# Performance work log

Measured on AMD Instinct MI355X. Metric: run time of the kernel, lower is better.

## Reference

```python
import jax, jax.numpy as jnp
import numpy as np

B, N, FIN, D1, D2 = 4096, 64, 256, 512, 128
NEG = -10000000.0


def setup_inputs() -> dict:
    key = jax.random.key(0)
    ks = jax.random.split(key, 12)
    s = lambda fan_in: 1.0 / np.sqrt(fan_in)
    return {
        "obs_x": jax.random.normal(ks[0], (B, FIN), jnp.float32),
        "others": jax.random.normal(ks[1], (B, N, FIN), jnp.float32),
        "action_mask": jax.random.randint(ks[2], (B, D2), 0, 2, jnp.int32),
        "W1": jax.random.normal(ks[3], (FIN, D1), jnp.float32) * s(FIN),
        "b1": jnp.zeros((D1,), jnp.float32),
        "W2": jax.random.normal(ks[4], (2 * D1, D2), jnp.float32) * s(2 * D1),
        "b2": jnp.zeros((D2,), jnp.float32),
        "W3": jax.random.normal(ks[5], (2 * D1, D2), jnp.float32) * s(2 * D1),
        "b3": jnp.zeros((D2,), jnp.float32),
        "W4": jax.random.normal(ks[6], (D2, 1), jnp.float32) * s(D2),
        "b4": jnp.zeros((1,), jnp.float32),
    }


def reference(obs_x, others, action_mask, W1, b1, W2, b2, W3, b3, W4, b4):
    # shared fc1 projection of self obs and other agents' obs
    x = obs_x @ W1 + b1                       # [B, D1]
    y = jnp.einsum("bnf,fd->bnd", others, W1) + b1  # [B, N, D1]
    # single-query dot-product attention over other agents
    alpha = jnp.einsum("bd,bnd->bn", x, y) / jnp.sqrt(jnp.float32(x.shape[-1]))
    beta = jax.nn.softmax(alpha, axis=-1)     # [B, N]
    c = jnp.einsum("bn,bnd->bd", beta, y)     # context [B, D1]
    out = jnp.concatenate([x, c], axis=-1)    # [B, 2*D1]
    out1 = jax.nn.softmax(out @ W2 + b2, axis=-1)  # policy branch (softmax then mask, as in source)
    mask = action_mask.astype(out1.dtype)
    logits = out1 + NEG * (1.0 - mask)
    value = (out @ W3 + b3) @ W4 + b4         # [B, 1] value head (stored as self._value_out)
    del value  # forward() returns only the masked logits
    return logits.reshape(-1, D2)
```

## Files before the change

kernel.cpp:

```cpp
#include <hip/hip_runtime.h>
#include <hip/hip_bf16.h>


typedef unsigned short u16;
typedef __bf16 bf16x8 __attribute__((ext_vector_type(8)));
typedef float f32x4 __attribute__((ext_vector_type(4)));

#define FIN 256
#define D1  512
#define D2  128
#define NNA 64
#define NEGV -10000000.0f

__device__ __forceinline__ float bf2f(u16 u) {
  unsigned int i = ((unsigned int)u) << 16;
  return __builtin_bit_cast(float, i);
}
__device__ __forceinline__ u16 f2bf(float f) {
  unsigned int i = __builtin_bit_cast(unsigned int, f);
  return (u16)((i + 0x7FFFu + ((i >> 16) & 1u)) >> 16);
}
__device__ __forceinline__ bf16x8 ld_frag_g(const u16* p) {
  return __builtin_bit_cast(bf16x8, *(const uint4*)p);
}
__device__ __forceinline__ bf16x8 ld_frag_f32(const float* p) {
  float4 a = *(const float4*)p, b = *(const float4*)(p + 4);
  u16 s[8];
  s[0] = f2bf(a.x); s[1] = f2bf(a.y); s[2] = f2bf(a.z); s[3] = f2bf(a.w);
  s[4] = f2bf(b.x); s[5] = f2bf(b.y); s[6] = f2bf(b.z); s[7] = f2bf(b.w);
  return __builtin_bit_cast(bf16x8, *(uint4*)s);
}

__global__ __launch_bounds__(256) void k_prep(const float* __restrict__ W1,
                                              const float* __restrict__ W2,
                                              u16* __restrict__ W1p,
                                              u16* __restrict__ W2p,
                                              u16* __restrict__ W1tp) {
  int tid = blockIdx.x * 256 + threadIdx.x;
  if (tid < 131072) {
    int idx = tid;
    int j = idx & 7, lane = (idx >> 3) & 63, nt = (idx >> 9) & 31, kt = idx >> 14;
    int k = kt * 32 + (lane >> 4) * 8 + j;
    int n = nt * 16 + (lane & 15);
    W1p[idx] = f2bf(W1[k * D1 + n]);
  } else if (tid < 163840) {
    int idx = tid - 131072;
    int j = idx & 7, lane = (idx >> 3) & 63, nt = (idx >> 9) & 7, kt = idx >> 12;
    int k = kt * 32 + (lane >> 4) * 8 + j;
    int n = nt * 16 + (lane & 15);
    W2p[idx] = f2bf(W2[k * D2 + n]);
  } else {
    int idx = tid - 163840;
    int j = idx & 7, lane = (idx >> 3) & 63, nt = (idx >> 9) & 15, kt = idx >> 13;
    int k = kt * 32 + (lane >> 4) * 8 + j;
    int n = nt * 16 + (lane & 15);
    W1tp[idx] = f2bf(W1[n * D1 + k]);
  }
}

__global__ __launch_bounds__(64) void k_x(const float* __restrict__ obs,
                                          const u16* __restrict__ W1p,
                                          const float* __restrict__ pb1,
                                          u16* __restrict__ outw) {
  const int lane = threadIdx.x & 63;
  const int q = lane >> 4, c0 = lane & 15;
  const int m0 = blockIdx.x * 32;
  const int ntg0 = blockIdx.y * 8;

  f32x4 acc[2][8];
#pragma unroll
  for (int a = 0; a < 2; ++a)
#pragma unroll
    for (int c = 0; c < 8; ++c) acc[a][c] = (f32x4){0.f, 0.f, 0.f, 0.f};

#pragma unroll 1
  for (int kt = 0; kt < 8; ++kt) {
    bf16x8 afr[2], bfr[8];
#pragma unroll
    for (int mt = 0; mt < 2; ++mt)
      afr[mt] = ld_frag_f32(obs + (m0 + mt * 16 + c0) * FIN + kt * 32 + q * 8);
#pragma unroll
    for (int nt = 0; nt < 8; ++nt)
      bfr[nt] = ld_frag_g(W1p + ((kt * 32 + ntg0 + nt) * 64 + lane) * 8);
#pragma unroll
    for (int mt = 0; mt < 2; ++mt)
#pragma unroll
      for (int nt = 0; nt < 8; ++nt)
        acc[mt][nt] = __builtin_amdgcn_mfma_f32_16x16x32_bf16(afr[mt], bfr[nt], acc[mt][nt], 0, 0, 0);
  }

#pragma unroll
  for (int nt = 0; nt < 8; ++nt) {
    const int n = (ntg0 + nt) * 16 + c0;
    const float bias = pb1[n];
#pragma unroll
    for (int mt = 0; mt < 2; ++mt)
#pragma unroll
      for (int i = 0; i < 4; ++i) {
        const int row = m0 + mt * 16 + q * 4 + i;
        outw[row * 512 + n] = f2bf(acc[mt][nt][i] + bias);
      }
  }
}

__global__ __launch_bounds__(64) void k_z(const u16* __restrict__ outw,
                                          const u16* __restrict__ W1tp,
                                          float* __restrict__ zbuf) {
  const int lane = threadIdx.x & 63;
  const int q = lane >> 4, c0 = lane & 15;
  const int m0 = blockIdx.x * 32;
  const int ntg0 = blockIdx.y * 8;

  f32x4 acc[2][8];
#pragma unroll
  for (int a = 0; a < 2; ++a)
#pragma unroll
    for (int c = 0; c < 8; ++c) acc[a][c] = (f32x4){0.f, 0.f, 0.f, 0.f};

#pragma unroll 1
  for (int kt = 0; kt < 16; ++kt) {
    bf16x8 afr[2], bfr[8];
#pragma unroll
    for (int mt = 0; mt < 2; ++mt)
      afr[mt] = ld_frag_g(outw + (m0 + mt * 16 + c0) * 512 + kt * 32 + q * 8);
#pragma unroll
    for (int nt = 0; nt < 8; ++nt)
      bfr[nt] = ld_frag_g(W1tp + ((kt * 16 + ntg0 + nt) * 64 + lane) * 8);
#pragma unroll
    for (int mt = 0; mt < 2; ++mt)
#pragma unroll
      for (int nt = 0; nt < 8; ++nt)
        acc[mt][nt] = __builtin_amdgcn_mfma_f32_16x16x32_bf16(afr[mt], bfr[nt], acc[mt][nt], 0, 0, 0);
  }

#pragma unroll
  for (int nt = 0; nt < 8; ++nt) {
    const int n = (ntg0 + nt) * 16 + c0;
#pragma unroll
    for (int mt = 0; mt < 2; ++mt)
#pragma unroll
      for (int i = 0; i < 4; ++i) {
        const int row = m0 + mt * 16 + q * 4 + i;
        zbuf[row * 256 + n] = acc[mt][nt][i];
      }
  }
}

__global__ __launch_bounds__(256, 4) void k_attn(const float* __restrict__ others,
                                                 const float* __restrict__ zbuf,
                                                 u16* __restrict__ obarb) {
  __shared__ float s_alpha[64];
  __shared__ float s_beta[64];
  __shared__ float s_part[1024];

  const int tid = threadIdx.x;
  const int b = blockIdx.x;
  const int w = tid >> 6, l = tid & 63;
  const float* src = others + (size_t)b * (NNA * FIN);

  const float4 z4 = *(const float4*)(zbuf + b * 256 + 4 * l);

  float4 o4[16];
#pragma unroll
  for (int r = 0; r < 16; ++r)
    o4[r] = *(const float4*)(src + (w * 16 + r) * 256 + 4 * l);

#pragma unroll
  for (int r = 0; r < 16; ++r) {
    float s = o4[r].x * z4.x + o4[r].y * z4.y + o4[r].z * z4.z + o4[r].w * z4.w;
    s += __shfl_xor(s, 1);  s += __shfl_xor(s, 2);  s += __shfl_xor(s, 4);
    s += __shfl_xor(s, 8);  s += __shfl_xor(s, 16); s += __shfl_xor(s, 32);
    if (l == r) s_alpha[w * 16 + r] = s * 0.04419417382415922f;
  }
  __syncthreads();

  if (tid < 64) {
    float v = s_alpha[tid];
    float mx = v;
#pragma unroll
    for (int off = 1; off < 64; off <<= 1) mx = fmaxf(mx, __shfl_xor(mx, off));
    float e = __expf(v - mx);
    float se = e;
#pragma unroll
    for (int off = 1; off < 64; off <<= 1) se += __shfl_xor(se, off);
    s_beta[tid] = e / se;
  }
  __syncthreads();

  float4 p = (float4){0.f, 0.f, 0.f, 0.f};
#pragma unroll
  for (int r = 0; r < 16; ++r) {
    const float bb = s_beta[w * 16 + r];
    p.x += bb * o4[r].x; p.y += bb * o4[r].y; p.z += bb * o4[r].z; p.w += bb * o4[r].w;
  }
  *(float4*)(&s_part[w * 256 + 4 * l]) = p;
  __syncthreads();

  const float v = s_part[tid] + s_part[tid + 256] + s_part[tid + 512] + s_part[tid + 768];
  obarb[(size_t)b * 256 + tid] = f2bf(v);
}

__global__ __launch_bounds__(128) void k_tail(const u16* __restrict__ outw,
                                              const u16* __restrict__ obarb,
                                              const u16* __restrict__ W1p,
                                              const float* __restrict__ pb1,
                                              const u16* __restrict__ W2p,
                                              const float* __restrict__ pb2,
                                              const int* __restrict__ mask,
                                              float* __restrict__ out) {
  __shared__ __align__(16) u16 c_s[16 * 520];
  __shared__ float s_mx[2][16];
  __shared__ float s_se[2][16];

  const int tid = threadIdx.x;
  const int w = tid >> 6, lane = tid & 63;
  const int q = lane >> 4, c0 = lane & 15;
  const int m0 = blockIdx.x * 16;

  {
    f32x4 acc[16];
#pragma unroll
    for (int c = 0; c < 16; ++c) acc[c] = (f32x4){0.f, 0.f, 0.f, 0.f};

#pragma unroll 1
    for (int kt = 0; kt < 8; ++kt) {
      bf16x8 afr = ld_frag_g(obarb + (m0 + c0) * 256 + kt * 32 + q * 8);
      bf16x8 bfr[16];
#pragma unroll
      for (int nt = 0; nt < 16; ++nt)
        bfr[nt] = ld_frag_g(W1p + ((kt * 32 + w * 16 + nt) * 64 + lane) * 8);
#pragma unroll
      for (int nt = 0; nt < 16; ++nt)
        acc[nt] = __builtin_amdgcn_mfma_f32_16x16x32_bf16(afr, bfr[nt], acc[nt], 0, 0, 0);
    }

#pragma unroll
    for (int nt = 0; nt < 16; ++nt) {
      const int n = w * 256 + nt * 16 + c0;
      const float bias = pb1[n];
#pragma unroll
      for (int i = 0; i < 4; ++i)
        c_s[(q * 4 + i) * 520 + n] = f2bf(acc[nt][i] + bias);
    }
  }
  __syncthreads();

  f32x4 acc[4];
#pragma unroll
  for (int c = 0; c < 4; ++c) acc[c] = (f32x4){0.f, 0.f, 0.f, 0.f};

#pragma unroll 1
  for (int kt = 0; kt < 16; ++kt) {
    bf16x8 afr = ld_frag_g(outw + (m0 + c0) * 512 + kt * 32 + q * 8);
    bf16x8 bfr[4];
#pragma unroll
    for (int nt = 0; nt < 4; ++nt)
      bfr[nt] = ld_frag_g(W2p + ((kt * 8 + w * 4 + nt) * 64 + lane) * 8);
#pragma unroll
    for (int nt = 0; nt < 4; ++nt)
      acc[nt] = __builtin_amdgcn_mfma_f32_16x16x32_bf16(afr, bfr[nt], acc[nt], 0, 0, 0);
  }
#pragma unroll 1
  for (int kt = 0; kt < 16; ++kt) {
    bf16x8 afr = __builtin_bit_cast(bf16x8, *(const uint4*)(c_s + c0 * 520 + kt * 32 + q * 8));
    bf16x8 bfr[4];
#pragma unroll
    for (int nt = 0; nt < 4; ++nt)
      bfr[nt] = ld_frag_g(W2p + (((kt + 16) * 8 + w * 4 + nt) * 64 + lane) * 8);
#pragma unroll
    for (int nt = 0; nt < 4; ++nt)
      acc[nt] = __builtin_amdgcn_mfma_f32_16x16x32_bf16(afr, bfr[nt], acc[nt], 0, 0, 0);
  }

  float b2f[4];
#pragma unroll
  for (int nt = 0; nt < 4; ++nt) b2f[nt] = pb2[(w * 4 + nt) * 16 + c0];

  float vv[4][4];
#pragma unroll
  for (int i = 0; i < 4; ++i) {
    float mx = -3.0e38f;
#pragma unroll
    for (int nt = 0; nt < 4; ++nt) { vv[i][nt] = acc[nt][i] + b2f[nt]; mx = fmaxf(mx, vv[i][nt]); }
    mx = fmaxf(mx, __shfl_xor(mx, 1)); mx = fmaxf(mx, __shfl_xor(mx, 2));
    mx = fmaxf(mx, __shfl_xor(mx, 4)); mx = fmaxf(mx, __shfl_xor(mx, 8));
    if (c0 == 0) s_mx[w][q * 4 + i] = mx;
  }
  __syncthreads();

#pragma unroll
  for (int i = 0; i < 4; ++i) {
    const int r = q * 4 + i;
    const float mx = fmaxf(s_mx[0][r], s_mx[1][r]);
    float se = 0.f;
#pragma unroll
    for (int nt = 0; nt < 4; ++nt) { vv[i][nt] = __expf(vv[i][nt] - mx); se += vv[i][nt]; }
    se += __shfl_xor(se, 1); se += __shfl_xor(se, 2);
    se += __shfl_xor(se, 4); se += __shfl_xor(se, 8);
    if (c0 == 0) s_se[w][q * 4 + i] = se;
  }
  __syncthreads();

#pragma unroll
  for (int i = 0; i < 4; ++i) {
    const int r = q * 4 + i;
    const int row = m0 + r;
    const float inv = 1.f / (s_se[0][r] + s_se[1][r]);
#pragma unroll
    for (int nt = 0; nt < 4; ++nt) {
      const int col = (w * 4 + nt) * 16 + c0;
      float p = fminf(fmaxf(vv[i][nt] * inv, 0.f), 1.f);
      float o = mask[row * D2 + col] ? p : (p + NEGV);
      out[row * D2 + col] = o;
    }
  }
}

extern "C" void kernel_launch(void* const* d_in, const int* in_sizes, int n_in,
                              void* d_out, int out_size, void* d_ws, size_t ws_size,
                              hipStream_t stream) {
  const float* obs = (const float*)d_in[0];
  const float* oth = (const float*)d_in[1];
  const int*   msk = (const int*)d_in[2];
  const float* W1  = (const float*)d_in[3];
  const float* b1  = (const float*)d_in[4];
  const float* W2  = (const float*)d_in[5];
  const float* b2  = (const float*)d_in[6];
  float* out = (float*)d_out;

  char* ws = (char*)d_ws;
  u16*   W1p   = (u16*)ws;
  u16*   W2p   = (u16*)(ws + 262144);
  u16*   W1tp  = (u16*)(ws + 327680);
  u16*   outw  = (u16*)(ws + 589824);
  float* zbuf  = (float*)(ws + 4784128);
  u16*   obarb = (u16*)(ws + 8978432);

  k_prep<<<1152, 256, 0, stream>>>(W1, W2, W1p, W2p, W1tp);
  k_x<<<dim3(128, 4), 64, 0, stream>>>(obs, W1p, b1, outw);
  k_z<<<dim3(128, 2), 64, 0, stream>>>(outw, W1tp, zbuf);
  k_attn<<<4096, 256, 0, stream>>>(oth, zbuf, obarb);
  k_tail<<<256, 128, 0, stream>>>(outw, obarb, W1p, b1, W2p, b2, msk, out);
}
```

Before: 427.2 us.

## Fuse x and z projections into one kernel and streamline attention reductions

Merges the x = obs@W1 and z = x@W1^T GEMMs into a single kernel. It keeps the bf16 x tile in shared memory so z no longer re-reads outw from global memory, and it saves one launch. In the attention kernel, the 16 separate full-wave shuffle reductions become a transposed butterfly reduction that needs far fewer shuffles. The others tensor is now read with nontemporal loads. The fused kernel uses 16-row tiles with 4 waves, which changes the parallelism and the reuse of W1 loads per block.

```diff
diff --git a/kernel.cpp b/kernel.cpp
--- a/kernel.cpp
+++ b/kernel.cpp
@@ -29,6 +29,9 @@
   s[0] = f2bf(a.x); s[1] = f2bf(a.y); s[2] = f2bf(a.z); s[3] = f2bf(a.w);
   s[4] = f2bf(b.x); s[5] = f2bf(b.y); s[6] = f2bf(b.z); s[7] = f2bf(b.w);
   return __builtin_bit_cast(bf16x8, *(uint4*)s);
+}
+__device__ __forceinline__ f32x4 ldnt(const float* p) {
+  return __builtin_nontemporal_load((const f32x4*)p);
 }
 
 __global__ __launch_bounds__(256) void k_prep(const float* __restrict__ W1,
@@ -58,91 +61,76 @@
   }
 }
 
-__global__ __launch_bounds__(64) void k_x(const float* __restrict__ obs,
-                                          const u16* __restrict__ W1p,
-                                          const float* __restrict__ pb1,
-                                          u16* __restrict__ outw) {
-  const int lane = threadIdx.x & 63;
+__global__ __launch_bounds__(256) void k_xz(const float* __restrict__ obs,
+                                            const u16* __restrict__ W1p,
+                                            const u16* __restrict__ W1tp,
+                                            const float* __restrict__ pb1,
+                                            u16* __restrict__ outw,
+                                            float* __restrict__ zbuf) {
+  __shared__ __align__(16) u16 x_s[16 * 520];
+
+  const int tid = threadIdx.x;
+  const int w = tid >> 6, lane = tid & 63;
   const int q = lane >> 4, c0 = lane & 15;
-  const int m0 = blockIdx.x * 32;
-  const int ntg0 = blockIdx.y * 8;
-
-  f32x4 acc[2][8];
-#pragma unroll
-  for (int a = 0; a < 2; ++a)
-#pragma unroll
-    for (int c = 0; c < 8; ++c) acc[a][c] = (f32x4){0.f, 0.f, 0.f, 0.f};
-
-#pragma unroll 1
-  for (int kt = 0; kt < 8; ++kt) {
-    bf16x8 afr[2], bfr[8];
-#pragma unroll
-    for (int mt = 0; mt < 2; ++mt)
-      afr[mt] = ld_frag_f32(obs + (m0 + mt * 16 + c0) * FIN + kt * 32 + q * 8);
-#pragma unroll
-    for (int nt = 0; nt < 8; ++nt)
-      bfr[nt] = ld_frag_g(W1p + ((kt * 32 + ntg0 + nt) * 64 + lane) * 8);
-#pragma unroll
-    for (int mt = 0; mt < 2; ++mt)
+  const int m0 = blockIdx.x * 16;
+  const int ntg0 = w * 8;
+
+  {
+    f32x4 acc[8];
+#pragma unroll
+    for (int c = 0; c < 8; ++c) acc[c] = (f32x4){0.f, 0.f, 0.f, 0.f};
+
+#pragma unroll 1
+    for (int kt = 0; kt < 8; ++kt) {
+      bf16x8 afr = ld_frag_f32(obs + (m0 + c0) * FIN + kt * 32 + q * 8);
+      bf16x8 bfr[8];
 #pragma unroll
       for (int nt = 0; nt < 8; ++nt)
-        acc[mt][nt] = __builtin_amdgcn_mfma_f32_16x16x32_bf16(afr[mt], bfr[nt], acc[mt][nt], 0, 0, 0);
-  }
-
-#pragma unroll
-  for (int nt = 0; nt < 8; ++nt) {
-    const int n = (ntg0 + nt) * 16 + c0;
-    const float bias = pb1[n];
-#pragma unroll
-    for (int mt = 0; mt < 2; ++mt)
+        bfr[nt] = ld_frag_g(W1p + ((kt * 32 + ntg0 + nt) * 64 + lane) * 8);
+#pragma unroll
+      for (int nt = 0; nt < 8; ++nt)
+        acc[nt] = __builtin_amdgcn_mfma_f32_16x16x32_bf16(afr, bfr[nt], acc[nt], 0, 0, 0);
+    }
+
+#pragma unroll
+    for (int nt = 0; nt < 8; ++nt) {
+      const int n = (ntg0 + nt) * 16 + c0;
+      const float bias = pb1[n];
 #pragma unroll
       for (int i = 0; i < 4; ++i) {
-        const int row = m0 + mt * 16 + q * 4 + i;
-        outw[row * 512 + n] = f2bf(acc[mt][nt][i] + bias);
+        const int r = q * 4 + i;
+        const u16 hv = f2bf(acc[nt][i] + bias);
+        outw[(m0 + r) * 512 + n] = hv;
+        x_s[r * 520 + n] = hv;
       }
-  }
-}
-
-__global__ __launch_bounds__(64) void k_z(const u16* __restrict__ outw,
-                                          const u16* __restrict__ W1tp,
-                                          float* __restrict__ zbuf) {
-  const int lane = threadIdx.x & 63;
-  const int q = lane >> 4, c0 = lane & 15;
-  const int m0 = blockIdx.x * 32;
-  const int ntg0 = blockIdx.y * 8;
-
-  f32x4 acc[2][8];
-#pragma unroll
-  for (int a = 0; a < 2; ++a)
-#pragma unroll
-    for (int c = 0; c < 8; ++c) acc[a][c] = (f32x4){0.f, 0.f, 0.f, 0.f};
-
-#pragma unroll 1
-  for (int kt = 0; kt < 16; ++kt) {
-    bf16x8 afr[2], bfr[8];
-#pragma unroll
-    for (int mt = 0; mt < 2; ++mt)
-      afr[mt] = ld_frag_g(outw + (m0 + mt * 16 + c0) * 512 + kt * 32 + q * 8);
-#pragma unroll
-    for (int nt = 0; nt < 8; ++nt)
-      bfr[nt] = ld_frag_g(W1tp + ((kt * 16 + ntg0 + nt) * 64 + lane) * 8);
-#pragma unroll
-    for (int mt = 0; mt < 2; ++mt)
-#pragma unroll
-      for (int nt = 0; nt < 8; ++nt)
-        acc[mt][nt] = __builtin_amdgcn_mfma_f32_16x16x32_bf16(afr[mt], bfr[nt], acc[mt][nt], 0, 0, 0);
-  }
-
-#pragma unroll
-  for (int nt = 0; nt < 8; ++nt) {
-    const int n = (ntg0 + nt) * 16 + c0;
-#pragma unroll
-    for (int mt = 0; mt < 2; ++mt)
-#pragma unroll
-      for (int i = 0; i < 4; ++i) {
-        const int row = m0 + mt * 16 + q * 4 + i;
-        zbuf[row * 256 + n] = acc[mt][nt][i];
-      }
+    }
+  }
+  __syncthreads();
+
+  {
+    f32x4 acc[4];
+#pragma unroll
+    for (int c = 0; c < 4; ++c) acc[c] = (f32x4){0.f, 0.f, 0.f, 0.f};
+
+#pragma unroll 1
+    for (int kt = 0; kt < 16; ++kt) {
+      bf16x8 afr = __builtin_bit_cast(bf16x8, *(const uint4*)(x_s + c0 * 520 + kt * 32 + q * 8));
+      bf16x8 bfr[4];
+#pragma unroll
+      for (int nt = 0; nt < 4; ++nt)
+        bfr[nt] = ld_frag_g(W1tp + ((kt * 16 + w * 4 + nt) * 64 + lane) * 8);
+#pragma unroll
+      for (int nt = 0; nt < 4; ++nt)
+        acc[nt] = __builtin_amdgcn_mfma_f32_16x16x32_bf16(afr, bfr[nt], acc[nt], 0, 0, 0);
+    }
+
+#pragma unroll
+    for (int nt = 0; nt < 4; ++nt) {
+      const int n = (w * 4 + nt) * 16 + c0;
+#pragma unroll
+      for (int i = 0; i < 4; ++i)
+        zbuf[(m0 + q * 4 + i) * 256 + n] = acc[nt][i];
+    }
   }
 }
 
@@ -158,28 +146,43 @@
   const int w = tid >> 6, l = tid & 63;
   const float* src = others + (size_t)b * (NNA * FIN);
 
-  const float4 z4 = *(const float4*)(zbuf + b * 256 + 4 * l);
-
-  float4 o4[16];
+  const f32x4 z4 = *(const f32x4*)(zbuf + b * 256 + 4 * l);
+
+  f32x4 o4[16];
 #pragma unroll
   for (int r = 0; r < 16; ++r)
-    o4[r] = *(const float4*)(src + (w * 16 + r) * 256 + 4 * l);
-
-#pragma unroll
-  for (int r = 0; r < 16; ++r) {
-    float s = o4[r].x * z4.x + o4[r].y * z4.y + o4[r].z * z4.z + o4[r].w * z4.w;
-    s += __shfl_xor(s, 1);  s += __shfl_xor(s, 2);  s += __shfl_xor(s, 4);
-    s += __shfl_xor(s, 8);  s += __shfl_xor(s, 16); s += __shfl_xor(s, 32);
-    if (l == r) s_alpha[w * 16 + r] = s * 0.04419417382415922f;
-  }
+    o4[r] = ldnt(src + (w * 16 + r) * 256 + 4 * l);
+
+  float v[16];
+#pragma unroll
+  for (int r = 0; r < 16; ++r)
+    v[r] = o4[r][0] * z4[0] + o4[r][1] * z4[1] + o4[r][2] * z4[2] + o4[r][3] * z4[3];
+
+#pragma unroll
+  for (int k = 0; k < 4; ++k) {
+    const int m = 1 << k;
+    const int half = 8 >> k;
+    const bool hi = (l & m) != 0;
+#pragma unroll
+    for (int i = 0; i < half; ++i) {
+      float a = v[i], bv = v[i + half];
+      float send = hi ? a : bv;
+      float keep = hi ? bv : a;
+      v[i] = keep + __shfl_xor(send, m);
+    }
+  }
+  v[0] += __shfl_xor(v[0], 16);
+  v[0] += __shfl_xor(v[0], 32);
+  const int rr = ((l & 1) << 3) | (((l >> 1) & 1) << 2) | (((l >> 2) & 1) << 1) | ((l >> 3) & 1);
+  if (l < 16) s_alpha[w * 16 + rr] = v[0] * 0.04419417382415922f;
   __syncthreads();
 
   if (tid < 64) {
-    float v = s_alpha[tid];
-    float mx = v;
+    float x = s_alpha[tid];
+    float mx = x;
 #pragma unroll
     for (int off = 1; off < 64; off <<= 1) mx = fmaxf(mx, __shfl_xor(mx, off));
-    float e = __expf(v - mx);
+    float e = __expf(x - mx);
     float se = e;
 #pragma unroll
     for (int off = 1; off < 64; off <<= 1) se += __shfl_xor(se, off);
@@ -187,17 +190,17 @@
   }
   __syncthreads();
 
-  float4 p = (float4){0.f, 0.f, 0.f, 0.f};
+  f32x4 p = (f32x4){0.f, 0.f, 0.f, 0.f};
 #pragma unroll
   for (int r = 0; r < 16; ++r) {
     const float bb = s_beta[w * 16 + r];
-    p.x += bb * o4[r].x; p.y += bb * o4[r].y; p.z += bb * o4[r].z; p.w += bb * o4[r].w;
-  }
-  *(float4*)(&s_part[w * 256 + 4 * l]) = p;
-  __syncthreads();
-
-  const float v = s_part[tid] + s_part[tid + 256] + s_part[tid + 512] + s_part[tid + 768];
-  obarb[(size_t)b * 256 + tid] = f2bf(v);
+    p[0] += bb * o4[r][0]; p[1] += bb * o4[r][1]; p[2] += bb * o4[r][2]; p[3] += bb * o4[r][3];
+  }
+  *(f32x4*)(&s_part[w * 256 + 4 * l]) = p;
+  __syncthreads();
+
+  const float vv = s_part[tid] + s_part[tid + 256] + s_part[tid + 512] + s_part[tid + 768];
+  obarb[(size_t)b * 256 + tid] = f2bf(vv);
 }
 
 __global__ __launch_bounds__(128) void k_tail(const u16* __restrict__ outw,
@@ -337,8 +340,7 @@
   u16*   obarb = (u16*)(ws + 8978432);
 
   k_prep<<<1152, 256, 0, stream>>>(W1, W2, W1p, W2p, W1tp);
-  k_x<<<dim3(128, 4), 64, 0, stream>>>(obs, W1p, b1, outw);
-  k_z<<<dim3(128, 2), 64, 0, stream>>>(outw, W1tp, zbuf);
+  k_xz<<<256, 256, 0, stream>>>(obs, W1p, W1tp, b1, outw, zbuf);
   k_attn<<<4096, 256, 0, stream>>>(oth, zbuf, obarb);
   k_tail<<<256, 128, 0, stream>>>(outw, obarb, W1p, b1, W2p, b2, msk, out);
 }
```

Result: faster. 391.5 us (-8.4%).
